# Kernel tuning notes

Measured on AMD Instinct MI355X. Metric: run time of the kernel, lower is better.

The kernel has to match this reference:

```python
import jax, jax.numpy as jnp
import numpy as np

D_MODEL = 1024
N_HEADS = 16
HEAD_DIM = D_MODEL // N_HEADS


def setup_inputs() -> dict:
    key = jax.random.key(0)
    ks = jax.random.split(key, 5)
    s_in = 1.0 / np.sqrt(D_MODEL)
    x = jax.random.normal(ks[0], (4, 2048, D_MODEL), dtype=jnp.float32)
    w_qkv = jax.random.uniform(ks[1], (3 * D_MODEL, D_MODEL), dtype=jnp.float32, minval=-s_in, maxval=s_in)
    b_qkv = jax.random.uniform(ks[2], (3 * D_MODEL,), dtype=jnp.float32, minval=-s_in, maxval=s_in)
    w_out = jax.random.uniform(ks[3], (D_MODEL, D_MODEL), dtype=jnp.float32, minval=-s_in, maxval=s_in)
    b_out = jax.random.uniform(ks[4], (D_MODEL,), dtype=jnp.float32, minval=-s_in, maxval=s_in)
    return {"x": x, "w_qkv": w_qkv, "b_qkv": b_qkv, "w_out": w_out, "b_out": b_out}


def reference(x, w_qkv, b_qkv, w_out, b_out):
    B, T, D = x.shape
    H, hd = N_HEADS, HEAD_DIM
    qkv = x @ w_qkv.T + b_qkv                      # [B, T, 3D]
    q, k, v = jnp.split(qkv, 3, axis=-1)
    # [B, H, T, hd]
    q = q.reshape(B, T, H, hd).transpose(0, 2, 1, 3)
    k = k.reshape(B, T, H, hd).transpose(0, 2, 1, 3)
    v = v.reshape(B, T, H, hd).transpose(0, 2, 1, 3)
    scale = 1.0 / np.sqrt(hd).astype(np.float32)
    attn = jnp.einsum('bhqd,bhkd->bhqk', q, k) * scale
    causal = jnp.triu(jnp.ones((T, T), dtype=bool), k=1)
    attn = jnp.where(causal, -jnp.inf, attn)
    attn = jax.nn.softmax(attn, axis=-1)
    out = jnp.einsum('bhqk,bhkd->bhqd', attn, v)
    out = out.transpose(0, 2, 1, 3).reshape(B, T, D)
    return out @ w_out.T + b_out
```

## Files before the change

### kernel.cpp

```cpp
#include <hip/hip_runtime.h>
#include <hip/hip_bf16.h>
#include <stdint.h>

#define D_MODEL 1024
#define NHEADS 16
#define HD 64
#define BB 4
#define TT 2048
#define MM (BB*TT)
#define NQKV (3*D_MODEL)
#define KK D_MODEL

typedef __attribute__((ext_vector_type(4))) float f32x4;
typedef __attribute__((ext_vector_type(8))) short bf16x8;

__device__ __forceinline__ unsigned short f2bf(float x){
    union { __hip_bfloat16 h; unsigned short u; } c;
    c.h = __float2bfloat16(x);
    return c.u;
}

__device__ __forceinline__ void gload_lds16(const void* g, void* l){
    __builtin_amdgcn_global_load_lds(
        (const __attribute__((address_space(1))) unsigned int*)g,
        (__attribute__((address_space(3))) unsigned int*)l,
        16, 0, 0);
}

#define N4_X  (MM*KK/4)
#define N4_WQ (NQKV*KK/4)
#define N4_WO (D_MODEL*D_MODEL/4)
__global__ void cast3_kernel(const float* __restrict__ x, const float* __restrict__ wq,
                             const float* __restrict__ wo,
                             unsigned short* __restrict__ xb, unsigned short* __restrict__ wqb,
                             unsigned short* __restrict__ wob){
    int i = blockIdx.x * blockDim.x + threadIdx.x;
    const float* src; unsigned short* dst; int j;
    if (i < N4_X)              { src = x;  dst = xb;  j = i; }
    else if (i < N4_X + N4_WQ) { src = wq; dst = wqb; j = i - N4_X; }
    else                       { src = wo; dst = wob; j = i - N4_X - N4_WQ; }
    float4 v = reinterpret_cast<const float4*>(src)[j];
    ushort4 o;
    o.x = f2bf(v.x); o.y = f2bf(v.y); o.z = f2bf(v.z); o.w = f2bf(v.w);
    reinterpret_cast<ushort4*>(dst)[j] = o;
}

__global__ __launch_bounds__(256) void gemm_qkv(
    const unsigned short* __restrict__ A, const unsigned short* __restrict__ Bw,
    const float* __restrict__ bias,
    unsigned short* __restrict__ qb, unsigned short* __restrict__ kb,
    unsigned short* __restrict__ vtb)
{
    __shared__ alignas(16) unsigned short As[2][128*32];
    __shared__ alignas(16) unsigned short Bs[2][128*32];
    const int tiles_n = NQKV/128;
    int nwg = gridDim.x;
    int orig = blockIdx.x;
    int bid = (orig & 7) * (nwg >> 3) + (orig >> 3);
    int bm = (bid / tiles_n) * 128;
    int bn = (bid % tiles_n) * 128;
    int tid = threadIdx.x;
    int w = tid >> 6, l = tid & 63;
    int wr = (w >> 1) * 64, wc = (w & 1) * 64;
    int lr = l & 15, hi = l >> 4;

    f32x4 acc[4][4] = {};

    int srow = tid >> 2;
    int scol = (tid & 3) * 8;
    const unsigned short* Ap = A + (size_t)(bm + srow) * KK + scol;
    const unsigned short* Bp = Bw + (size_t)(bn + srow) * KK + scol;

    {
        char* AsB = (char*)&As[0][0] + w*1024;
        char* BsB = (char*)&Bs[0][0] + w*1024;
        gload_lds16(Ap,           AsB);
        gload_lds16(Ap + 64*KK,   AsB + 4096);
        gload_lds16(Bp,           BsB);
        gload_lds16(Bp + 64*KK,   BsB + 4096);
    }
    __syncthreads();

    int cur = 0;
    for (int k0 = 0; k0 < KK; k0 += 32) {
        if (k0 + 32 < KK) {
            char* AsB = (cur ? (char*)&As[0][0] : (char*)&As[1][0]) + w*1024;
            char* BsB = (cur ? (char*)&Bs[0][0] : (char*)&Bs[1][0]) + w*1024;
            gload_lds16(Ap + k0 + 32,          AsB);
            gload_lds16(Ap + 64*KK + k0 + 32,  AsB + 4096);
            gload_lds16(Bp + k0 + 32,          BsB);
            gload_lds16(Bp + 64*KK + k0 + 32,  BsB + 4096);
        }
        const unsigned short* Ab = cur ? &As[1][0] : &As[0][0];
        const unsigned short* Bb = cur ? &Bs[1][0] : &Bs[0][0];
        bf16x8 af[4], bfr[4];
        #pragma unroll
        for (int m = 0; m < 4; m++)
            af[m] = *reinterpret_cast<const bf16x8*>(&Ab[(wr + m*16 + lr)*32 + hi*8]);
        #pragma unroll
        for (int n = 0; n < 4; n++)
            bfr[n] = *reinterpret_cast<const bf16x8*>(&Bb[(wc + n*16 + lr)*32 + hi*8]);
        #pragma unroll
        for (int m = 0; m < 4; m++)
            #pragma unroll
            for (int n = 0; n < 4; n++)
                acc[m][n] = __builtin_amdgcn_mfma_f32_16x16x32_bf16(af[m], bfr[n], acc[m][n], 0, 0, 0);
        __syncthreads();
        cur ^= 1;
    }

    #pragma unroll
    for (int m = 0; m < 4; m++) {
        int gm = bm + wr + m*16 + hi*4;
        int b  = gm >> 11;
        int t  = gm & 2047;
        #pragma unroll
        for (int n = 0; n < 4; n++) {
            int gn = bn + wc + n*16 + lr;
            float bv = bias[gn];
            int sec = gn >> 10;
            int nn  = gn & 1023;
            int h = nn >> 6, d = nn & 63;
            int bh = b * NHEADS + h;
            if (sec == 2) {
                ushort4 pk;
                pk.x = f2bf(acc[m][n][0] + bv);
                pk.y = f2bf(acc[m][n][1] + bv);
                pk.z = f2bf(acc[m][n][2] + bv);
                pk.w = f2bf(acc[m][n][3] + bv);
                *reinterpret_cast<ushort4*>(&vtb[((size_t)bh*HD + d)*TT + t]) = pk;
            } else {
                unsigned short* dst = (sec == 0) ? qb : kb;
                #pragma unroll
                for (int r = 0; r < 4; r++)
                    dst[((size_t)bh*TT + t + r)*HD + d] = f2bf(acc[m][n][r] + bv);
            }
        }
    }
}

__global__ __launch_bounds__(512) void attn_kernel(
    const unsigned short* __restrict__ qb, const unsigned short* __restrict__ kb,
    const unsigned short* __restrict__ vtb, unsigned short* __restrict__ ao)
{
    __shared__ alignas(16) unsigned short Kb[2][64*64];
    __shared__ alignas(16) unsigned short Vb[2][64*64];
    __shared__ alignas(16) unsigned short Pl[8][16*64];

    const int bh = blockIdx.x;
    const int qt = (gridDim.y - 1) - blockIdx.y;
    const int tid = threadIdx.x;
    const int w = tid >> 6, l = tid & 63;
    const int lr = l & 15, hi = l >> 4;

    const int qbase = qt * 128;
    const int qrow  = qbase + w*16;
    const int ktmax = 2*qt + 1;

    const unsigned short* Qp = qb + ((size_t)bh*TT + qrow) * HD;
    bf16x8 qf0 = *reinterpret_cast<const bf16x8*>(Qp + lr*HD + hi*8);
    bf16x8 qf1 = *reinterpret_cast<const bf16x8*>(Qp + lr*HD + 32 + hi*8);

    const unsigned short* Kg = kb  + (size_t)bh*TT*HD;
    const unsigned short* Vg = vtb + (size_t)bh*HD*TT;

    const int srow = w*8 + (l >> 3);
    const int sc16 = (l & 7) ^ (srow & 7);
    char* KbL0 = (char*)&Kb[0][0] + w*1024;
    char* KbL1 = (char*)&Kb[1][0] + w*1024;
    char* VbL0 = (char*)&Vb[0][0] + w*1024;
    char* VbL1 = (char*)&Vb[1][0] + w*1024;

    gload_lds16(Kg + (size_t)srow*HD + sc16*8, KbL0);
    gload_lds16(Vg + (size_t)srow*TT + sc16*8, VbL0);
    __syncthreads();

    float mS = -3e38f, lS = 0.f;
    f32x4 o[4] = {};
    const float sc = 0.125f * 1.4426950408889634f;
    const float THR = 8.0f / sc;
    const int qg = qrow + lr;
    const int swp = (lr & 7) << 4;
    char* Pw = (char*)&Pl[w][0];

    int cur = 0;
    for (int kt = 0; kt <= ktmax; ++kt) {
        const int kbase = kt*64;
        if (kt < ktmax) {
            int knext = kbase + 64;
            char* kd = cur ? KbL0 : KbL1;
            char* vd = cur ? VbL0 : VbL1;
            gload_lds16(Kg + (size_t)(knext + srow)*HD + sc16*8, kd);
            gload_lds16(Vg + (size_t)srow*TT + knext + sc16*8,   vd);
        }
        if (kbase <= qrow + 15) {
            const char* Kl = cur ? (const char*)&Kb[1][0] : (const char*)&Kb[0][0];
            const char* Vl = cur ? (const char*)&Vb[1][0] : (const char*)&Vb[0][0];
            f32x4 s[4] = {};
            __builtin_amdgcn_s_setprio(1);
            #pragma unroll
            for (int n = 0; n < 4; n++) {
                int rb = (n*16 + lr) * 128;
                bf16x8 kf0 = *reinterpret_cast<const bf16x8*>(Kl + rb + (( 0 + hi*16) ^ swp));
                bf16x8 kf1 = *reinterpret_cast<const bf16x8*>(Kl + rb + ((64 + hi*16) ^ swp));
                s[n] = __builtin_amdgcn_mfma_f32_16x16x32_bf16(kf0, qf0, s[n], 0, 0, 0);
                s[n] = __builtin_amdgcn_mfma_f32_16x16x32_bf16(kf1, qf1, s[n], 0, 0, 0);
            }
            __builtin_amdgcn_s_setprio(0);
            if (kbase + 63 > qrow) {
                #pragma unroll
                for (int n = 0; n < 4; n++)
                    #pragma unroll
                    for (int r = 0; r < 4; r++)
                        if (kbase + n*16 + hi*4 + r > qg) s[n][r] = -3e38f;
            }
            float t0 = fmaxf(fmaxf(s[0][0], s[0][1]), fmaxf(s[0][2], s[0][3]));
            float t1 = fmaxf(fmaxf(s[1][0], s[1][1]), fmaxf(s[1][2], s[1][3]));
            float t2 = fmaxf(fmaxf(s[2][0], s[2][1]), fmaxf(s[2][2], s[2][3]));
            float t3 = fmaxf(fmaxf(s[3][0], s[3][1]), fmaxf(s[3][2], s[3][3]));
            float rm = fmaxf(fmaxf(t0, t1), fmaxf(t2, t3));
            rm = fmaxf(rm, __shfl_xor(rm, 16, 64));
            rm = fmaxf(rm, __shfl_xor(rm, 32, 64));
            if (!__all(rm - mS <= THR)) {
                float newm = fmaxf(mS, rm);
                float al = exp2f(sc * (mS - newm));
                mS = newm;
                lS *= al;
                #pragma unroll
                for (int r = 0; r < 4; r++) {
                    float alr = __shfl(al, hi*4 + r, 64);
                    o[0][r] *= alr; o[1][r] *= alr; o[2][r] *= alr; o[3][r] *= alr;
                }
            }
            const float c0 = sc * mS;
            float rs = 0.f;
            #pragma unroll
            for (int n = 0; n < 4; n++) {
                float p0 = exp2f(fmaf(s[n][0], sc, -c0));
                float p1 = exp2f(fmaf(s[n][1], sc, -c0));
                float p2 = exp2f(fmaf(s[n][2], sc, -c0));
                float p3 = exp2f(fmaf(s[n][3], sc, -c0));
                rs += (p0 + p1) + (p2 + p3);
                ushort4 u;
                u.x = f2bf(p0); u.y = f2bf(p1); u.z = f2bf(p2); u.w = f2bf(p3);
                *reinterpret_cast<ushort4*>(Pw + (lr*128 + ((n*32 + hi*8) ^ swp))) = u;
            }
            rs += __shfl_xor(rs, 16, 64);
            rs += __shfl_xor(rs, 32, 64);
            lS += rs;
            bf16x8 pa0 = *reinterpret_cast<const bf16x8*>(Pw + (lr*128 + (( 0 + hi*16) ^ swp)));
            bf16x8 pa1 = *reinterpret_cast<const bf16x8*>(Pw + (lr*128 + ((64 + hi*16) ^ swp)));
            __builtin_amdgcn_s_setprio(1);
            #pragma unroll
            for (int nd = 0; nd < 4; nd++) {
                int rb = (nd*16 + lr) * 128;
                bf16x8 vf0 = *reinterpret_cast<const bf16x8*>(Vl + rb + (( 0 + hi*16) ^ swp));
                bf16x8 vf1 = *reinterpret_cast<const bf16x8*>(Vl + rb + ((64 + hi*16) ^ swp));
                o[nd] = __builtin_amdgcn_mfma_f32_16x16x32_bf16(pa0, vf0, o[nd], 0, 0, 0);
                o[nd] = __builtin_amdgcn_mfma_f32_16x16x32_bf16(pa1, vf1, o[nd], 0, 0, 0);
            }
            __builtin_amdgcn_s_setprio(0);
        }
        __syncthreads();
        cur ^= 1;
    }

    float inv = 1.0f / lS;
    int b = bh >> 4, h = bh & 15;
    #pragma unroll
    for (int r = 0; r < 4; r++) {
        float invr = __shfl(inv, hi*4 + r, 64);
        int t = qrow + hi*4 + r;
        #pragma unroll
        for (int nd = 0; nd < 4; nd++) {
            float val = o[nd][r] * invr;
            ao[((size_t)b*TT + t)*D_MODEL + h*HD + nd*16 + lr] = f2bf(val);
        }
    }
}

__global__ __launch_bounds__(256) void gemm_out(
    const unsigned short* __restrict__ A, const unsigned short* __restrict__ Bw,
    const float* __restrict__ bias, float* __restrict__ out)
{
    __shared__ alignas(16) unsigned short As[2][128*32];
    __shared__ alignas(16) unsigned short Bs[2][128*32];
    const int tiles_n = D_MODEL/128;
    int nwg = gridDim.x;
    int orig = blockIdx.x;
    int bid = (orig & 7) * (nwg >> 3) + (orig >> 3);
    int bm = (bid / tiles_n) * 128;
    int bn = (bid % tiles_n) * 128;
    int tid = threadIdx.x;
    int w = tid >> 6, l = tid & 63;
    int wr = (w >> 1) * 64, wc = (w & 1) * 64;
    int lr = l & 15, hi = l >> 4;

    f32x4 acc[4][4] = {};

    int srow = tid >> 2;
    int scol = (tid & 3) * 8;
    const unsigned short* Ap = A + (size_t)(bm + srow) * KK + scol;
    const unsigned short* Bp = Bw + (size_t)(bn + srow) * KK + scol;

    {
        char* AsB = (char*)&As[0][0] + w*1024;
        char* BsB = (char*)&Bs[0][0] + w*1024;
        gload_lds16(Ap,           AsB);
        gload_lds16(Ap + 64*KK,   AsB + 4096);
        gload_lds16(Bp,           BsB);
        gload_lds16(Bp + 64*KK,   BsB + 4096);
    }
    __syncthreads();

    int cur = 0;
    for (int k0 = 0; k0 < KK; k0 += 32) {
        if (k0 + 32 < KK) {
            char* AsB = (cur ? (char*)&As[0][0] : (char*)&As[1][0]) + w*1024;
            char* BsB = (cur ? (char*)&Bs[0][0] : (char*)&Bs[1][0]) + w*1024;
            gload_lds16(Ap + k0 + 32,          AsB);
            gload_lds16(Ap + 64*KK + k0 + 32,  AsB + 4096);
            gload_lds16(Bp + k0 + 32,          BsB);
            gload_lds16(Bp + 64*KK + k0 + 32,  BsB + 4096);
        }
        const unsigned short* Ab = cur ? &As[1][0] : &As[0][0];
        const unsigned short* Bb = cur ? &Bs[1][0] : &Bs[0][0];
        bf16x8 af[4], bfr[4];
        #pragma unroll
        for (int m = 0; m < 4; m++)
            af[m] = *reinterpret_cast<const bf16x8*>(&Ab[(wr + m*16 + lr)*32 + hi*8]);
        #pragma unroll
        for (int n = 0; n < 4; n++)
            bfr[n] = *reinterpret_cast<const bf16x8*>(&Bb[(wc + n*16 + lr)*32 + hi*8]);
        #pragma unroll
        for (int m = 0; m < 4; m++)
            #pragma unroll
            for (int n = 0; n < 4; n++)
                acc[m][n] = __builtin_amdgcn_mfma_f32_16x16x32_bf16(af[m], bfr[n], acc[m][n], 0, 0, 0);
        __syncthreads();
        cur ^= 1;
    }

    #pragma unroll
    for (int m = 0; m < 4; m++) {
        int gm = bm + wr + m*16 + hi*4;
        #pragma unroll
        for (int n = 0; n < 4; n++) {
            int gn = bn + wc + n*16 + lr;
            float bv = bias[gn];
            #pragma unroll
            for (int r = 0; r < 4; r++)
                out[(size_t)(gm + r)*D_MODEL + gn] = acc[m][n][r] + bv;
        }
    }
}

extern "C" void kernel_launch(void* const* d_in, const int* in_sizes, int n_in,
                              void* d_out, int out_size, void* d_ws, size_t ws_size,
                              hipStream_t stream) {
    const float* x     = (const float*)d_in[0];
    const float* w_qkv = (const float*)d_in[1];
    const float* b_qkv = (const float*)d_in[2];
    const float* w_out = (const float*)d_in[3];
    const float* b_out = (const float*)d_in[4];
    float* out = (float*)d_out;

    char* ws = (char*)d_ws;
    unsigned short* xbf   = (unsigned short*)(ws);
    unsigned short* wqkvb = (unsigned short*)(ws + (size_t)16777216);
    unsigned short* woutb = (unsigned short*)(ws + (size_t)23068672);
    unsigned short* qb    = (unsigned short*)(ws + (size_t)25165824);
    unsigned short* kb    = (unsigned short*)(ws + (size_t)41943040);
    unsigned short* vtb   = (unsigned short*)(ws + (size_t)58720256);
    unsigned short* aob   = xbf;

    cast3_kernel<<<(N4_X + N4_WQ + N4_WO)/256, 256, 0, stream>>>(x, w_qkv, w_out, xbf, wqkvb, woutb);

    gemm_qkv<<<(MM/128)*(NQKV/128), 256, 0, stream>>>(xbf, wqkvb, b_qkv, qb, kb, vtb);
    attn_kernel<<<dim3(BB*NHEADS, TT/128), 512, 0, stream>>>(qb, kb, vtb, aob);
    gemm_out<<<(MM/128)*(D_MODEL/128), 256, 0, stream>>>(aob, woutb, b_out, out);
}
```

Measured before the change: 179.9 us.

## Process two K/V tiles per iteration with a single combined softmax rescale

```diff
diff --git a/kernel.cpp b/kernel.cpp
--- a/kernel.cpp
+++ b/kernel.cpp
@@ -143,8 +143,8 @@
     const unsigned short* __restrict__ qb, const unsigned short* __restrict__ kb,
     const unsigned short* __restrict__ vtb, unsigned short* __restrict__ ao)
 {
-    __shared__ alignas(16) unsigned short Kb[2][64*64];
-    __shared__ alignas(16) unsigned short Vb[2][64*64];
+    __shared__ alignas(16) unsigned short Kt[4][64*64];
+    __shared__ alignas(16) unsigned short Vt[4][64*64];
     __shared__ alignas(16) unsigned short Pl[8][16*64];
 
     const int bh = blockIdx.x;
@@ -155,7 +155,7 @@
 
     const int qbase = qt * 128;
     const int qrow  = qbase + w*16;
-    const int ktmax = 2*qt + 1;
+    const int npairs = qt + 1;
 
     const unsigned short* Qp = qb + ((size_t)bh*TT + qrow) * HD;
     bf16x8 qf0 = *reinterpret_cast<const bf16x8*>(Qp + lr*HD + hi*8);
@@ -166,13 +166,15 @@
 
     const int srow = w*8 + (l >> 3);
     const int sc16 = (l & 7) ^ (srow & 7);
-    char* KbL0 = (char*)&Kb[0][0] + w*1024;
-    char* KbL1 = (char*)&Kb[1][0] + w*1024;
-    char* VbL0 = (char*)&Vb[0][0] + w*1024;
-    char* VbL1 = (char*)&Vb[1][0] + w*1024;
-
-    gload_lds16(Kg + (size_t)srow*HD + sc16*8, KbL0);
-    gload_lds16(Vg + (size_t)srow*TT + sc16*8, VbL0);
+    char* KS0 = (char*)&Kt[0][0] + w*1024;  char* KS1 = (char*)&Kt[1][0] + w*1024;
+    char* KS2 = (char*)&Kt[2][0] + w*1024;  char* KS3 = (char*)&Kt[3][0] + w*1024;
+    char* VS0 = (char*)&Vt[0][0] + w*1024;  char* VS1 = (char*)&Vt[1][0] + w*1024;
+    char* VS2 = (char*)&Vt[2][0] + w*1024;  char* VS3 = (char*)&Vt[3][0] + w*1024;
+
+    gload_lds16(Kg + (size_t)srow*HD + sc16*8,        KS0);
+    gload_lds16(Vg + (size_t)srow*TT + sc16*8,        VS0);
+    gload_lds16(Kg + (size_t)(64 + srow)*HD + sc16*8, KS1);
+    gload_lds16(Vg + (size_t)srow*TT + 64 + sc16*8,   VS1);
     __syncthreads();
 
     float mS = -3e38f, lS = 0.f;
@@ -183,86 +185,150 @@
     const int swp = (lr & 7) << 4;
     char* Pw = (char*)&Pl[w][0];
 
-    int cur = 0;
-    for (int kt = 0; kt <= ktmax; ++kt) {
-        const int kbase = kt*64;
-        if (kt < ktmax) {
-            int knext = kbase + 64;
-            char* kd = cur ? KbL0 : KbL1;
-            char* vd = cur ? VbL0 : VbL1;
-            gload_lds16(Kg + (size_t)(knext + srow)*HD + sc16*8, kd);
-            gload_lds16(Vg + (size_t)srow*TT + knext + sc16*8,   vd);
-        }
-        if (kbase <= qrow + 15) {
-            const char* Kl = cur ? (const char*)&Kb[1][0] : (const char*)&Kb[0][0];
-            const char* Vl = cur ? (const char*)&Vb[1][0] : (const char*)&Vb[0][0];
-            f32x4 s[4] = {};
-            __builtin_amdgcn_s_setprio(1);
+    for (int j = 0; j < npairs; ++j) {
+        const int ph = j & 1;
+        const char* Ka = ph ? (const char*)&Kt[2][0] : (const char*)&Kt[0][0];
+        const char* Kc = ph ? (const char*)&Kt[3][0] : (const char*)&Kt[1][0];
+        const char* Va = ph ? (const char*)&Vt[2][0] : (const char*)&Vt[0][0];
+        const char* Vc = ph ? (const char*)&Vt[3][0] : (const char*)&Vt[1][0];
+        if (j + 1 < npairs) {
+            const int tn = 2*j + 2;
+            char* kd0 = ph ? KS0 : KS2;  char* kd1 = ph ? KS1 : KS3;
+            char* vd0 = ph ? VS0 : VS2;  char* vd1 = ph ? VS1 : VS3;
+            gload_lds16(Kg + (size_t)(tn*64 + srow)*HD + sc16*8,      kd0);
+            gload_lds16(Vg + (size_t)srow*TT + tn*64 + sc16*8,        vd0);
+            gload_lds16(Kg + (size_t)(tn*64 + 64 + srow)*HD + sc16*8, kd1);
+            gload_lds16(Vg + (size_t)srow*TT + tn*64 + 64 + sc16*8,   vd1);
+        }
+        const int kba = 2*j*64;
+        const int kbb = kba + 64;
+        const bool cb = (kbb <= qrow + 15);
+
+        f32x4 sa4[4] = {}, sb4[4] = {};
+        __builtin_amdgcn_s_setprio(1);
+        #pragma unroll
+        for (int n = 0; n < 4; n++) {
+            int rb = (n*16 + lr) * 128;
+            bf16x8 k0 = *reinterpret_cast<const bf16x8*>(Ka + rb + (( 0 + hi*16) ^ swp));
+            bf16x8 k1 = *reinterpret_cast<const bf16x8*>(Ka + rb + ((64 + hi*16) ^ swp));
+            sa4[n] = __builtin_amdgcn_mfma_f32_16x16x32_bf16(k0, qf0, sa4[n], 0, 0, 0);
+            sa4[n] = __builtin_amdgcn_mfma_f32_16x16x32_bf16(k1, qf1, sa4[n], 0, 0, 0);
+        }
+        if (cb) {
             #pragma unroll
             for (int n = 0; n < 4; n++) {
                 int rb = (n*16 + lr) * 128;
-                bf16x8 kf0 = *reinterpret_cast<const bf16x8*>(Kl + rb + (( 0 + hi*16) ^ swp));
-                bf16x8 kf1 = *reinterpret_cast<const bf16x8*>(Kl + rb + ((64 + hi*16) ^ swp));
-                s[n] = __builtin_amdgcn_mfma_f32_16x16x32_bf16(kf0, qf0, s[n], 0, 0, 0);
-                s[n] = __builtin_amdgcn_mfma_f32_16x16x32_bf16(kf1, qf1, s[n], 0, 0, 0);
-            }
-            __builtin_amdgcn_s_setprio(0);
-            if (kbase + 63 > qrow) {
+                bf16x8 k0 = *reinterpret_cast<const bf16x8*>(Kc + rb + (( 0 + hi*16) ^ swp));
+                bf16x8 k1 = *reinterpret_cast<const bf16x8*>(Kc + rb + ((64 + hi*16) ^ swp));
+                sb4[n] = __builtin_amdgcn_mfma_f32_16x16x32_bf16(k0, qf0, sb4[n], 0, 0, 0);
+                sb4[n] = __builtin_amdgcn_mfma_f32_16x16x32_bf16(k1, qf1, sb4[n], 0, 0, 0);
+            }
+        }
+        __builtin_amdgcn_s_setprio(0);
+
+        if (kba + 63 > qrow) {
+            #pragma unroll
+            for (int n = 0; n < 4; n++)
                 #pragma unroll
-                for (int n = 0; n < 4; n++)
-                    #pragma unroll
-                    for (int r = 0; r < 4; r++)
-                        if (kbase + n*16 + hi*4 + r > qg) s[n][r] = -3e38f;
-            }
-            float t0 = fmaxf(fmaxf(s[0][0], s[0][1]), fmaxf(s[0][2], s[0][3]));
-            float t1 = fmaxf(fmaxf(s[1][0], s[1][1]), fmaxf(s[1][2], s[1][3]));
-            float t2 = fmaxf(fmaxf(s[2][0], s[2][1]), fmaxf(s[2][2], s[2][3]));
-            float t3 = fmaxf(fmaxf(s[3][0], s[3][1]), fmaxf(s[3][2], s[3][3]));
-            float rm = fmaxf(fmaxf(t0, t1), fmaxf(t2, t3));
-            rm = fmaxf(rm, __shfl_xor(rm, 16, 64));
-            rm = fmaxf(rm, __shfl_xor(rm, 32, 64));
-            if (!__all(rm - mS <= THR)) {
-                float newm = fmaxf(mS, rm);
-                float al = exp2f(sc * (mS - newm));
-                mS = newm;
-                lS *= al;
+                for (int r = 0; r < 4; r++)
+                    if (kba + n*16 + hi*4 + r > qg) sa4[n][r] = -3e38f;
+        }
+        if (cb && kbb + 63 > qrow) {
+            #pragma unroll
+            for (int n = 0; n < 4; n++)
                 #pragma unroll
-                for (int r = 0; r < 4; r++) {
-                    float alr = __shfl(al, hi*4 + r, 64);
-                    o[0][r] *= alr; o[1][r] *= alr; o[2][r] *= alr; o[3][r] *= alr;
-                }
-            }
-            const float c0 = sc * mS;
-            float rs = 0.f;
+                for (int r = 0; r < 4; r++)
+                    if (kbb + n*16 + hi*4 + r > qg) sb4[n][r] = -3e38f;
+        }
+
+        float t0 = fmaxf(fmaxf(sa4[0][0], sa4[0][1]), fmaxf(sa4[0][2], sa4[0][3]));
+        float t1 = fmaxf(fmaxf(sa4[1][0], sa4[1][1]), fmaxf(sa4[1][2], sa4[1][3]));
+        float t2 = fmaxf(fmaxf(sa4[2][0], sa4[2][1]), fmaxf(sa4[2][2], sa4[2][3]));
+        float t3 = fmaxf(fmaxf(sa4[3][0], sa4[3][1]), fmaxf(sa4[3][2], sa4[3][3]));
+        float rm = fmaxf(fmaxf(t0, t1), fmaxf(t2, t3));
+        if (cb) {
+            float u0 = fmaxf(fmaxf(sb4[0][0], sb4[0][1]), fmaxf(sb4[0][2], sb4[0][3]));
+            float u1 = fmaxf(fmaxf(sb4[1][0], sb4[1][1]), fmaxf(sb4[1][2], sb4[1][3]));
+            float u2 = fmaxf(fmaxf(sb4[2][0], sb4[2][1]), fmaxf(sb4[2][2], sb4[2][3]));
+            float u3 = fmaxf(fmaxf(sb4[3][0], sb4[3][1]), fmaxf(sb4[3][2], sb4[3][3]));
+            rm = fmaxf(rm, fmaxf(fmaxf(u0, u1), fmaxf(u2, u3)));
+        }
+        rm = fmaxf(rm, __shfl_xor(rm, 16, 64));
+        rm = fmaxf(rm, __shfl_xor(rm, 32, 64));
+        if (!__all(rm - mS <= THR)) {
+            float newm = fmaxf(mS, rm);
+            float al = exp2f(sc * (mS - newm));
+            mS = newm;
+            lS *= al;
+            #pragma unroll
+            for (int r = 0; r < 4; r++) {
+                float alr = __shfl(al, hi*4 + r, 64);
+                o[0][r] *= alr; o[1][r] *= alr; o[2][r] *= alr; o[3][r] *= alr;
+            }
+        }
+        const float c0 = sc * mS;
+
+        float rs = 0.f;
+        #pragma unroll
+        for (int n = 0; n < 4; n++) {
+            float p0 = exp2f(fmaf(sa4[n][0], sc, -c0));
+            float p1 = exp2f(fmaf(sa4[n][1], sc, -c0));
+            float p2 = exp2f(fmaf(sa4[n][2], sc, -c0));
+            float p3 = exp2f(fmaf(sa4[n][3], sc, -c0));
+            rs += (p0 + p1) + (p2 + p3);
+            ushort4 u;
+            u.x = f2bf(p0); u.y = f2bf(p1); u.z = f2bf(p2); u.w = f2bf(p3);
+            *reinterpret_cast<ushort4*>(Pw + (lr*128 + ((n*32 + hi*8) ^ swp))) = u;
+        }
+        ushort4 ub[4];
+        if (cb) {
             #pragma unroll
             for (int n = 0; n < 4; n++) {
-                float p0 = exp2f(fmaf(s[n][0], sc, -c0));
-                float p1 = exp2f(fmaf(s[n][1], sc, -c0));
-                float p2 = exp2f(fmaf(s[n][2], sc, -c0));
-                float p3 = exp2f(fmaf(s[n][3], sc, -c0));
+                float p0 = exp2f(fmaf(sb4[n][0], sc, -c0));
+                float p1 = exp2f(fmaf(sb4[n][1], sc, -c0));
+                float p2 = exp2f(fmaf(sb4[n][2], sc, -c0));
+                float p3 = exp2f(fmaf(sb4[n][3], sc, -c0));
                 rs += (p0 + p1) + (p2 + p3);
-                ushort4 u;
-                u.x = f2bf(p0); u.y = f2bf(p1); u.z = f2bf(p2); u.w = f2bf(p3);
-                *reinterpret_cast<ushort4*>(Pw + (lr*128 + ((n*32 + hi*8) ^ swp))) = u;
-            }
-            rs += __shfl_xor(rs, 16, 64);
-            rs += __shfl_xor(rs, 32, 64);
-            lS += rs;
+                ub[n].x = f2bf(p0); ub[n].y = f2bf(p1);
+                ub[n].z = f2bf(p2); ub[n].w = f2bf(p3);
+            }
+        }
+        rs += __shfl_xor(rs, 16, 64);
+        rs += __shfl_xor(rs, 32, 64);
+        lS += rs;
+
+        {
             bf16x8 pa0 = *reinterpret_cast<const bf16x8*>(Pw + (lr*128 + (( 0 + hi*16) ^ swp)));
             bf16x8 pa1 = *reinterpret_cast<const bf16x8*>(Pw + (lr*128 + ((64 + hi*16) ^ swp)));
             __builtin_amdgcn_s_setprio(1);
             #pragma unroll
             for (int nd = 0; nd < 4; nd++) {
                 int rb = (nd*16 + lr) * 128;
-                bf16x8 vf0 = *reinterpret_cast<const bf16x8*>(Vl + rb + (( 0 + hi*16) ^ swp));
-                bf16x8 vf1 = *reinterpret_cast<const bf16x8*>(Vl + rb + ((64 + hi*16) ^ swp));
-                o[nd] = __builtin_amdgcn_mfma_f32_16x16x32_bf16(pa0, vf0, o[nd], 0, 0, 0);
-                o[nd] = __builtin_amdgcn_mfma_f32_16x16x32_bf16(pa1, vf1, o[nd], 0, 0, 0);
+                bf16x8 v0 = *reinterpret_cast<const bf16x8*>(Va + rb + (( 0 + hi*16) ^ swp));
+                bf16x8 v1 = *reinterpret_cast<const bf16x8*>(Va + rb + ((64 + hi*16) ^ swp));
+                o[nd] = __builtin_amdgcn_mfma_f32_16x16x32_bf16(pa0, v0, o[nd], 0, 0, 0);
+                o[nd] = __builtin_amdgcn_mfma_f32_16x16x32_bf16(pa1, v1, o[nd], 0, 0, 0);
             }
             __builtin_amdgcn_s_setprio(0);
         }
+        if (cb) {
+            #pragma unroll
+            for (int n = 0; n < 4; n++)
+                *reinterpret_cast<ushort4*>(Pw + (lr*128 + ((n*32 + hi*8) ^ swp))) = ub[n];
+            bf16x8 pa0 = *reinterpret_cast<const bf16x8*>(Pw + (lr*128 + (( 0 + hi*16) ^ swp)));
+            bf16x8 pa1 = *reinterpret_cast<const bf16x8*>(Pw + (lr*128 + ((64 + hi*16) ^ swp)));
+            __builtin_amdgcn_s_setprio(1);
+            #pragma unroll
+            for (int nd = 0; nd < 4; nd++) {
+                int rb = (nd*16 + lr) * 128;
+                bf16x8 v0 = *reinterpret_cast<const bf16x8*>(Vc + rb + (( 0 + hi*16) ^ swp));
+                bf16x8 v1 = *reinterpret_cast<const bf16x8*>(Vc + rb + ((64 + hi*16) ^ swp));
+                o[nd] = __builtin_amdgcn_mfma_f32_16x16x32_bf16(pa0, v0, o[nd], 0, 0, 0);
+                o[nd] = __builtin_amdgcn_mfma_f32_16x16x32_bf16(pa1, v1, o[nd], 0, 0, 0);
+            }
+            __builtin_amdgcn_s_setprio(0);
+        }
         __syncthreads();
-        cur ^= 1;
     }
 
     float inv = 1.0f / lS;
```

Measured after the change: 177.9 us. No clear change (-1.1%).
